# Optimization experiments

Hardware: AMD Instinct MI355X
Metric: run time of the kernel (lower is better)

Reference implementation:

```python
import jax, jax.numpy as jnp
import numpy as np

NUM_EXPERTS = 8
TOP_K = 2


def setup_inputs() -> dict:
    key = jax.random.key(0)
    k0, k1, k2, k3, k4 = jax.random.split(key, 5)
    sl, bs, hs, ffn = 2048, 2, 512, 2048
    T = sl * bs
    x = jax.random.normal(k0, (sl, bs, hs), jnp.float32)
    expert_weights = jax.random.uniform(k1, (T, TOP_K), jnp.float32)
    expert_indices = jax.random.randint(k2, (T, TOP_K), 0, NUM_EXPERTS)
    # per-expert MLP params (ParallelGroupedMLP, 'regular' mlp_type)
    w1 = jax.random.normal(k3, (NUM_EXPERTS, hs, ffn), jnp.float32) * (hs ** -0.5)
    w2 = jax.random.normal(k4, (NUM_EXPERTS, ffn, hs), jnp.float32) * (ffn ** -0.5)
    return dict(x=x, expert_weights=expert_weights, expert_indices=expert_indices, w1=w1, w2=w2)


def reference(x, expert_weights, expert_indices, w1, w2):
    """Dropless MoE: sort assignments by expert, gather tokens, grouped MLP,
    scatter-combine with top-k router weights (megablocks gather/scatter semantics)."""
    in_shape = x.shape
    hs = in_shape[-1]
    x_flat = x.reshape(-1, hs)                 # [T, hs]
    T = x_flat.shape[0]
    flat_ids = expert_indices.reshape(-1)      # [T*k] expert id per assignment
    order = jnp.argsort(flat_ids)              # indices: assignment order sorted by expert
    bin_ids = flat_ids[order]                  # expert id per sorted slot
    token_ids = order // TOP_K                 # source token per sorted slot
    xg = x_flat[token_ids]                     # gather: [T*k, hs]
    # grouped GEMM: fixed small loop over experts, mask-select per slot
    y = jnp.zeros_like(xg)
    for e in range(NUM_EXPERTS):
        h = jax.nn.gelu(xg @ w1[e], approximate=False)   # [T*k, ffn]
        y = jnp.where((bin_ids == e)[:, None], h @ w2[e], y)
    # scatter-combine: out[token] += weight[assignment] * y[slot]
    w = expert_weights.reshape(-1)[order][:, None]       # [T*k, 1]
    out = jnp.zeros((T, hs), x.dtype).at[token_ids].add(w * y)
    return out.reshape(in_shape)
```

## Files before the change

### kernel.cpp

```cpp
#include <hip/hip_runtime.h>
#include <stdint.h>

#define T_TOK 4096
#define KTOP  2
#define HS    512
#define FFN   2048
#define NE    8
#define NA    (T_TOK*KTOP)
#define MT    128
#define BK    64
#define MT_MAX 72
#define SLOT_CAP (MT_MAX*MT)
#define PSTR 68
#define NB_G1 576

#define MB_ (1024ull*1024ull)
#define WS_OFF   1024u
#define WS_MEXP  1088u
#define WS_SLOTS 2048u
#define WS_INV   40960u
#define WS_XB   (1*MB_)
#define WS_W1T  (5*MB_)
#define WS_W2T  (21*MB_)
#define WS_HB   (37*MB_)
#define WS_YPB0 (73*MB_)
#define WS_YPB1 (82*MB_)
#define WS_NEED (91*MB_)

typedef short bf16x8 __attribute__((ext_vector_type(8)));
typedef float f32x4  __attribute__((ext_vector_type(4)));

__device__ __forceinline__ unsigned short f2bf(float f) {
    unsigned u = __builtin_bit_cast(unsigned, f);
    u += 0x7fffu + ((u >> 16) & 1u);
    return (unsigned short)(u >> 16);
}
__device__ __forceinline__ float bf2f(unsigned short h) {
    return __builtin_bit_cast(float, (unsigned)h << 16);
}
__device__ __forceinline__ float gelu_fast(float x) {
    float x2 = x * x;
    float inner = fmaf(0.044715f * x2, x, x);
    float E = __expf(1.5957691216057308f * inner);
    return x - x / (1.0f + E);
}
__device__ __forceinline__ void gl_lds16(const void* g, void* l) {
    __builtin_amdgcn_global_load_lds(
        (const __attribute__((address_space(1))) unsigned int*)g,
        (__attribute__((address_space(3))) unsigned int*)l, 16, 0, 0);
}

__device__ __forceinline__ void transpose_cvt64(
    const float* __restrict__ src, unsigned short* __restrict__ dh,
    int R, int C, int e, int kb, int nb, int t, float (*tile)[65])
{
    const int k0 = kb * 64, n0 = nb * 64;
    #pragma unroll
    for (int q = 0; q < 4; ++q) {
        int f4 = t + q * 256;
        int kk = f4 >> 4, nn4 = f4 & 15;
        float4 v = *reinterpret_cast<const float4*>(
            &src[((size_t)e * R + k0 + kk) * C + n0 + nn4 * 4]);
        tile[kk][nn4 * 4 + 0] = v.x; tile[kk][nn4 * 4 + 1] = v.y;
        tile[kk][nn4 * 4 + 2] = v.z; tile[kk][nn4 * 4 + 3] = v.w;
    }
    __syncthreads();
    #pragma unroll
    for (int q = 0; q < 4; ++q) {
        int wid = t + q * 256;
        int nn = wid >> 4, kk4 = wid & 15;
        ushort4 o;
        o.x = f2bf(tile[kk4 * 4 + 0][nn]);
        o.y = f2bf(tile[kk4 * 4 + 1][nn]);
        o.z = f2bf(tile[kk4 * 4 + 2][nn]);
        o.w = f2bf(tile[kk4 * 4 + 3][nn]);
        *reinterpret_cast<ushort4*>(&dh[((size_t)e * C + n0 + nn) * R + k0 + kk4 * 4]) = o;
    }
}

__global__ void moe_prep1(const int* __restrict__ eidx,
                          int* slots, int* inv, int* offp, int* mexp,
                          const float* __restrict__ x, unsigned short* __restrict__ xb,
                          const float* __restrict__ w1, unsigned short* __restrict__ w1t)
{
    __shared__ float tile[64][65];
    const int bid = blockIdx.x, t = threadIdx.x;
    if (bid < 2048) {
        int i = bid * 256 + t;
        float4 v = reinterpret_cast<const float4*>(x)[i];
        uint2 p = { (unsigned)f2bf(v.x) | ((unsigned)f2bf(v.y) << 16),
                    (unsigned)f2bf(v.z) | ((unsigned)f2bf(v.w) << 16) };
        reinterpret_cast<uint2*>(xb)[i] = p;
    } else if (bid < 4096) {
        int lin = bid - 2048, e = lin >> 8, rem = lin & 255;
        transpose_cvt64(w1, w1t, HS, FFN, e, rem & 7, rem >> 3, t, tile);
    } else {
        __shared__ int hfull[NE], hpre[NE], elocal[256];
        __shared__ int off_l[NE + 1];
        const int f = bid - 4096;
        if (t < NE) { hfull[t] = 0; hpre[t] = 0; }
        __syncthreads();
        const int base = f * 256;
        for (int i = t; i < NA; i += 256) {
            int ee = eidx[i];
            atomicAdd(&hfull[ee], 1);
            if (i < base) atomicAdd(&hpre[ee], 1);
        }
        if (f < 32) elocal[t] = eidx[base + t];
        __syncthreads();
        if (t == 0) {
            int run = 0;
            for (int q = 0; q < NE; ++q) { off_l[q] = run; run += ((hfull[q] + MT - 1) / MT) * MT; }
            off_l[NE] = run;
        }
        __syncthreads();
        if (f < 32) {
            int a = base + t, e = elocal[t];
            int rank = 0;
            for (int j = 0; j < t; ++j) rank += (elocal[j] == e) ? 1 : 0;
            int s = off_l[e] + hpre[e] + rank;
            slots[s] = a;
            inv[a] = s;
        } else {
            for (int e = 0; e < NE; ++e)
                for (int s = off_l[e] + hfull[e] + t; s < off_l[e + 1]; s += 256)
                    slots[s] = -1;
            for (int s = off_l[NE] + t; s < SLOT_CAP; s += 256) slots[s] = -1;
            if (t <= NE) offp[t] = off_l[t];
            if (t < MT_MAX) {
                int m0 = t * MT, ee = 0;
                #pragma unroll
                for (int q = 0; q < NE; ++q)
                    if (m0 >= off_l[q] && m0 < off_l[q + 1]) ee = q;
                mexp[t] = ee;
            }
        }
    }
}

__global__ __launch_bounds__(256, 2) void moe_g1w2(
    const unsigned short* __restrict__ XB, const unsigned short* __restrict__ W1T,
    const int* __restrict__ offp, const int* __restrict__ mexp,
    const int* __restrict__ slots, unsigned short* __restrict__ HB,
    const float* __restrict__ w2, unsigned short* __restrict__ w2t)
{
    __shared__ __align__(16) char POOL[49152];
    __shared__ int srow[MT];
    const int t = threadIdx.x;

    if (blockIdx.x >= NB_G1) {
        int lin = blockIdx.x - NB_G1;
        int e = lin >> 8, rem = lin & 255;
        transpose_cvt64(w2, w2t, FFN, HS, e, rem & 31, rem >> 5, t,
                        reinterpret_cast<float(*)[65]>(POOL));
        return;
    }

    const int xcd = blockIdx.x & 7;
    const int part = blockIdx.x >> 3;
    const int mtg = part % 9;
    const int nt  = part / 9;
    const int mt  = xcd * 9 + mtg;
    if (mt * MT >= offp[NE]) return;
    const int e = mexp[mt];
    const int lane = t & 63, wv = t >> 6;

    short* As = (short*)POOL;
    short* Bs = (short*)(POOL + 16384);
    float* Pf = (float*)POOL;

    if (t < MT) { int s = slots[mt * MT + t]; srow[t] = (s < 0) ? 0 : (s >> 1); }
    __syncthreads();

    int baseA[4], baseB[8];
    #pragma unroll
    for (int q = 0; q < 4; ++q) {
        int i = wv * 4 + q;
        int row = i * 8 + (lane >> 3);
        int sg = (lane & 7) ^ (row & 7);
        baseA[q] = srow[row] * HS + sg * 8;
    }
    #pragma unroll
    for (int q = 0; q < 8; ++q) {
        int j = wv * 8 + q;
        int row = j * 8 + (lane >> 3);
        int sg = (lane & 7) ^ (row & 7);
        baseB[q] = (e * FFN + nt * 256 + row) * HS + sg * 8;
    }

    const int wm = wv >> 1, wn = wv & 1, q4 = lane >> 4, l15 = lane & 15;
    int offA[2][4], offB[2][8];
    #pragma unroll
    for (int m = 0; m < 4; ++m) {
        int r = wm * 64 + m * 16 + l15;
        #pragma unroll
        for (int ks = 0; ks < 2; ++ks)
            offA[ks][m] = r * 128 + ((((ks << 2) | q4) ^ (r & 7)) << 4);
    }
    #pragma unroll
    for (int n = 0; n < 8; ++n) {
        int rb = wn * 128 + n * 16 + l15;
        #pragma unroll
        for (int ks = 0; ks < 2; ++ks)
            offB[ks][n] = rb * 128 + ((((ks << 2) | q4) ^ (rb & 7)) << 4);
    }

    f32x4 acc[4][8];
    #pragma unroll
    for (int m = 0; m < 4; ++m)
        #pragma unroll
        for (int n = 0; n < 8; ++n) { f32x4 z = {0.f, 0.f, 0.f, 0.f}; acc[m][n] = z; }

    for (int kk = 0; kk < HS; kk += BK) {
        __syncthreads();
        #pragma unroll
        for (int q = 0; q < 4; ++q)
            gl_lds16(XB + baseA[q] + kk, (char*)As + (wv * 4 + q) * 1024);
        #pragma unroll
        for (int q = 0; q < 8; ++q)
            gl_lds16(W1T + baseB[q] + kk, (char*)Bs + (wv * 8 + q) * 1024);
        __syncthreads();
        #pragma unroll
        for (int ks = 0; ks < 2; ++ks) {
            bf16x8 a[4], b[8];
            #pragma unroll
            for (int m = 0; m < 4; ++m)
                a[m] = *(const bf16x8*)((const char*)As + offA[ks][m]);
            #pragma unroll
            for (int n = 0; n < 8; ++n)
                b[n] = *(const bf16x8*)((const char*)Bs + offB[ks][n]);
            #pragma unroll
            for (int m = 0; m < 4; ++m)
                #pragma unroll
                for (int n = 0; n < 8; ++n)
                    acc[m][n] = __builtin_amdgcn_mfma_f32_16x16x32_bf16(a[m], b[n], acc[m][n], 0, 0, 0);
        }
    }

    #pragma unroll
    for (int qq = 0; qq < 4; ++qq) {
        const int wn_q = qq >> 1, nq = (qq & 1) * 4;
        __syncthreads();
        if (wn == wn_q) {
            #pragma unroll
            for (int m = 0; m < 4; ++m)
                #pragma unroll
                for (int nn = 0; nn < 4; ++nn)
                    #pragma unroll
                    for (int j = 0; j < 4; ++j)
                        Pf[(wm * 64 + m * 16 + q4 * 4 + j) * PSTR + nn * 16 + l15] = acc[m][nq + nn][j];
        }
        __syncthreads();
        #pragma unroll
        for (int q = 0; q < 4; ++q) {
            int seg = q * 256 + t, row = seg >> 3, c8 = (seg & 7) << 3;
            const float* p = Pf + row * PSTR + c8;
            float4 a = *(const float4*)p, b = *(const float4*)(p + 4);
            float va[8] = {a.x, a.y, a.z, a.w, b.x, b.y, b.z, b.w};
            bf16x8 ph;
            #pragma unroll
            for (int i = 0; i < 8; ++i) ph[i] = (short)f2bf(gelu_fast(va[i]));
            *(bf16x8*)(HB + (size_t)(mt * MT + row) * FFN + nt * 256 + qq * 64 + c8) = ph;
        }
    }
}

__global__ __launch_bounds__(256, 4) void moe_gemm2(
    const unsigned short* __restrict__ HB, const unsigned short* __restrict__ W2T,
    const int* __restrict__ offp, const int* __restrict__ mexp,
    unsigned short* __restrict__ YPB0, unsigned short* __restrict__ YPB1)
{
    const int xcd = blockIdx.x & 7;
    const int part = blockIdx.x >> 3;
    const int sub = part % 8;
    const int mtg = part / 8;
    const int mt  = xcd * 9 + mtg;
    const int nt  = sub >> 1, kpart = sub & 1;
    if (mt * MT >= offp[NE]) return;
    const int e = mexp[mt];
    const int t = threadIdx.x, lane = t & 63, wv = t >> 6;

    __shared__ __align__(16) char POOL[MT * PSTR * 4];
    short* As = (short*)POOL;
    short* Bs = (short*)(POOL + 16384);
    float* Pf = (float*)POOL;

    int baseA[4], baseB[4];
    #pragma unroll
    for (int q = 0; q < 4; ++q) {
        int i = wv * 4 + q;
        int row = i * 8 + (lane >> 3);
        int sg = (lane & 7) ^ (row & 7);
        baseA[q] = (mt * MT + row) * FFN + sg * 8;
        baseB[q] = (e * HS + nt * MT + row) * FFN + sg * 8;
    }

    const int wm = wv >> 1, wn = wv & 1, q4 = lane >> 4, l15 = lane & 15;
    int offA[2][4], offB[2][4];
    #pragma unroll
    for (int m = 0; m < 4; ++m) {
        int r  = wm * 64 + m * 16 + l15;
        int rb = wn * 64 + m * 16 + l15;
        #pragma unroll
        for (int ks = 0; ks < 2; ++ks) {
            offA[ks][m] = r  * 128 + ((((ks << 2) | q4) ^ (r  & 7)) << 4);
            offB[ks][m] = rb * 128 + ((((ks << 2) | q4) ^ (rb & 7)) << 4);
        }
    }

    f32x4 acc[4][4];
    #pragma unroll
    for (int m = 0; m < 4; ++m)
        #pragma unroll
        for (int n = 0; n < 4; ++n) { f32x4 z = {0.f, 0.f, 0.f, 0.f}; acc[m][n] = z; }

    const int k0 = kpart * (FFN / 2), k1 = k0 + FFN / 2;
    for (int kk = k0; kk < k1; kk += BK) {
        __syncthreads();
        #pragma unroll
        for (int q = 0; q < 4; ++q) {
            int i = wv * 4 + q;
            gl_lds16(HB  + baseA[q] + kk, (char*)As + i * 1024);
            gl_lds16(W2T + baseB[q] + kk, (char*)Bs + i * 1024);
        }
        __syncthreads();
        #pragma unroll
        for (int ks = 0; ks < 2; ++ks) {
            bf16x8 a[4], b[4];
            #pragma unroll
            for (int m = 0; m < 4; ++m) {
                a[m] = *(const bf16x8*)((const char*)As + offA[ks][m]);
                b[m] = *(const bf16x8*)((const char*)Bs + offB[ks][m]);
            }
            #pragma unroll
            for (int m = 0; m < 4; ++m)
                #pragma unroll
                for (int n = 0; n < 4; ++n)
                    acc[m][n] = __builtin_amdgcn_mfma_f32_16x16x32_bf16(a[m], b[n], acc[m][n], 0, 0, 0);
        }
    }

    unsigned short* YP = kpart ? YPB1 : YPB0;
    #pragma unroll
    for (int half = 0; half < 2; ++half) {
        __syncthreads();
        if (wn == half) {
            #pragma unroll
            for (int m = 0; m < 4; ++m)
                #pragma unroll
                for (int n = 0; n < 4; ++n)
                    #pragma unroll
                    for (int j = 0; j < 4; ++j)
                        Pf[(wm * 64 + m * 16 + q4 * 4 + j) * PSTR + n * 16 + l15] = acc[m][n][j];
        }
        __syncthreads();
        #pragma unroll
        for (int q = 0; q < 4; ++q) {
            int seg = q * 256 + t, row = seg >> 3, c8 = (seg & 7) << 3;
            const float* p = Pf + row * PSTR + c8;
            float4 a = *(const float4*)p, b = *(const float4*)(p + 4);
            float va[8] = {a.x, a.y, a.z, a.w, b.x, b.y, b.z, b.w};
            bf16x8 ph;
            #pragma unroll
            for (int i = 0; i < 8; ++i) ph[i] = (short)f2bf(va[i]);
            *(bf16x8*)(YP + (size_t)(mt * MT + row) * HS + nt * MT + half * 64 + c8) = ph;
        }
    }
}

__global__ void moe_combine2(const unsigned short* __restrict__ YPB0,
                             const unsigned short* __restrict__ YPB1,
                             const int* __restrict__ inv, const float* __restrict__ ew,
                             float* __restrict__ out) {
    int i = blockIdx.x * 256 + threadIdx.x;
    if (i >= T_TOK * HS / 8) return;
    int tk = i >> 6, c8 = (i & 63) << 3;
    int s0 = inv[2 * tk], s1 = inv[2 * tk + 1];
    float w0 = ew[2 * tk], w1 = ew[2 * tk + 1];
    bf16x8 a0 = *(const bf16x8*)(YPB0 + (size_t)s0 * HS + c8);
    bf16x8 b0 = *(const bf16x8*)(YPB1 + (size_t)s0 * HS + c8);
    bf16x8 a1 = *(const bf16x8*)(YPB0 + (size_t)s1 * HS + c8);
    bf16x8 b1 = *(const bf16x8*)(YPB1 + (size_t)s1 * HS + c8);
    float o[8];
    #pragma unroll
    for (int j = 0; j < 8; ++j)
        o[j] = w0 * (bf2f((unsigned short)a0[j]) + bf2f((unsigned short)b0[j]))
             + w1 * (bf2f((unsigned short)a1[j]) + bf2f((unsigned short)b1[j]));
    float4* d = reinterpret_cast<float4*>(out + (size_t)i * 8);
    d[0] = make_float4(o[0], o[1], o[2], o[3]);
    d[1] = make_float4(o[4], o[5], o[6], o[7]);
}

#define FB_BM 32
#define FB_BJ 128
#define FB_CK 256
#define FB_XSTR (FB_CK+4)
#define FB_HSTR (FB_BJ+4)

__device__ __forceinline__ float fb_gelu(float v) {
    return 0.5f * v * (1.0f + erff(v * 0.70710678118654752f));
}

__global__ void fb_init(int* cnt) { int i = threadIdx.x; if (i < NE) cnt[i] = 0; }

__global__ void fb_scatter(const int* __restrict__ eidx, int* cnt, int* bucket) {
    int a = blockIdx.x * 256 + threadIdx.x;
    if (a < NA) { int e = eidx[a]; int p = atomicAdd(&cnt[e], 1); bucket[e * NA + p] = a; }
}

__global__ __launch_bounds__(256, 1) void fb_fused(
    const float* __restrict__ x, const float* __restrict__ w1, const float* __restrict__ w2,
    const int* __restrict__ cnt, const int* __restrict__ bucket, float* __restrict__ ybuf)
{
    const int bid = blockIdx.x;
    const int e = bid & (NE - 1), tr = bid >> 3;
    const int n_e = cnt[e], rbase = tr * FB_BM;
    if (rbase >= n_e) return;
    const int t = threadIdx.x;
    __shared__ __align__(16) float Xc[FB_BM][FB_XSTR];
    __shared__ __align__(16) float Hsh[FB_BM][FB_HSTR];
    __shared__ int rowa[FB_BM];
    if (t < FB_BM) { int r = rbase + t; rowa[t] = (r < n_e) ? bucket[e * NA + r] : -1; }
    __syncthreads();
    const int cg = t & 15, rg = t >> 4, r0 = rg * 2;
    float yac[2][32];
    #pragma unroll
    for (int u = 0; u < 2; ++u)
        #pragma unroll
        for (int v = 0; v < 32; ++v) yac[u][v] = 0.0f;
    const float* w1e = w1 + (size_t)e * HS * FFN;
    const float* w2e = w2 + (size_t)e * FFN * HS;
    for (int jp = 0; jp < FFN; jp += FB_BJ) {
        float hac[2][8];
        #pragma unroll
        for (int u = 0; u < 2; ++u)
            #pragma unroll
            for (int v = 0; v < 8; ++v) hac[u][v] = 0.0f;
        for (int ic = 0; ic < HS; ic += FB_CK) {
            __syncthreads();
            #pragma unroll
            for (int q = 0; q < (FB_BM * FB_CK / 4) / 256; ++q) {
                int id = t + 256 * q, rr = id >> 6, c4 = id & 63;
                int a = rowa[rr];
                float4 val = make_float4(0.f, 0.f, 0.f, 0.f);
                if (a >= 0) val = *reinterpret_cast<const float4*>(x + (size_t)(a >> 1) * HS + ic + c4 * 4);
                *reinterpret_cast<float4*>(&Xc[rr][c4 * 4]) = val;
            }
            __syncthreads();
            const float* w1p = w1e + (size_t)ic * FFN + jp + cg * 8;
            #pragma unroll 2
            for (int i4 = 0; i4 < FB_CK; i4 += 4) {
                float4 xa = *reinterpret_cast<const float4*>(&Xc[r0][i4]);
                float4 xb = *reinterpret_cast<const float4*>(&Xc[r0 + 1][i4]);
                const float* wr0 = w1p + (size_t)i4 * FFN;
                #pragma unroll
                for (int ii = 0; ii < 4; ++ii) {
                    float4 wa = *reinterpret_cast<const float4*>(wr0 + (size_t)ii * FFN);
                    float4 wb = *reinterpret_cast<const float4*>(wr0 + (size_t)ii * FFN + 4);
                    float x0 = (ii == 0) ? xa.x : (ii == 1) ? xa.y : (ii == 2) ? xa.z : xa.w;
                    float x1 = (ii == 0) ? xb.x : (ii == 1) ? xb.y : (ii == 2) ? xb.z : xb.w;
                    hac[0][0] = fmaf(x0, wa.x, hac[0][0]); hac[0][1] = fmaf(x0, wa.y, hac[0][1]);
                    hac[0][2] = fmaf(x0, wa.z, hac[0][2]); hac[0][3] = fmaf(x0, wa.w, hac[0][3]);
                    hac[0][4] = fmaf(x0, wb.x, hac[0][4]); hac[0][5] = fmaf(x0, wb.y, hac[0][5]);
                    hac[0][6] = fmaf(x0, wb.z, hac[0][6]); hac[0][7] = fmaf(x0, wb.w, hac[0][7]);
                    hac[1][0] = fmaf(x1, wa.x, hac[1][0]); hac[1][1] = fmaf(x1, wa.y, hac[1][1]);
                    hac[1][2] = fmaf(x1, wa.z, hac[1][2]); hac[1][3] = fmaf(x1, wa.w, hac[1][3]);
                    hac[1][4] = fmaf(x1, wb.x, hac[1][4]); hac[1][5] = fmaf(x1, wb.y, hac[1][5]);
                    hac[1][6] = fmaf(x1, wb.z, hac[1][6]); hac[1][7] = fmaf(x1, wb.w, hac[1][7]);
                }
            }
        }
        #pragma unroll
        for (int u = 0; u < 2; ++u)
            #pragma unroll
            for (int v = 0; v < 8; ++v) Hsh[r0 + u][cg * 8 + v] = fb_gelu(hac[u][v]);
        __syncthreads();
        const float* w2p = w2e + (size_t)jp * HS + cg * 32;
        #pragma unroll 2
        for (int j = 0; j < FB_BJ; ++j) {
            float h0 = Hsh[r0][j], h1 = Hsh[r0 + 1][j];
            const float* wr = w2p + (size_t)j * HS;
            #pragma unroll
            for (int q = 0; q < 8; ++q) {
                float4 w4 = *reinterpret_cast<const float4*>(wr + q * 4);
                yac[0][q * 4 + 0] = fmaf(h0, w4.x, yac[0][q * 4 + 0]);
                yac[0][q * 4 + 1] = fmaf(h0, w4.y, yac[0][q * 4 + 1]);
                yac[0][q * 4 + 2] = fmaf(h0, w4.z, yac[0][q * 4 + 2]);
                yac[0][q * 4 + 3] = fmaf(h0, w4.w, yac[0][q * 4 + 3]);
                yac[1][q * 4 + 0] = fmaf(h1, w4.x, yac[1][q * 4 + 0]);
                yac[1][q * 4 + 1] = fmaf(h1, w4.y, yac[1][q * 4 + 1]);
                yac[1][q * 4 + 2] = fmaf(h1, w4.z, yac[1][q * 4 + 2]);
                yac[1][q * 4 + 3] = fmaf(h1, w4.w, yac[1][q * 4 + 3]);
            }
        }
    }
    #pragma unroll
    for (int u = 0; u < 2; ++u) {
        int a = rowa[r0 + u];
        if (a >= 0) {
            float* yp = ybuf + (size_t)a * HS + cg * 32;
            #pragma unroll
            for (int q = 0; q < 8; ++q) {
                float4 o = make_float4(yac[u][q * 4 + 0], yac[u][q * 4 + 1],
                                       yac[u][q * 4 + 2], yac[u][q * 4 + 3]);
                *reinterpret_cast<float4*>(yp + q * 4) = o;
            }
        }
    }
}

__global__ void fb_combine(const float* __restrict__ ybuf, const float* __restrict__ ew,
                           float* __restrict__ out) {
    int i = blockIdx.x * 256 + threadIdx.x;
    if (i >= T_TOK * HS / 4) return;
    int tk = i >> 7, c4 = i & 127;
    float wA = ew[2 * tk], wB = ew[2 * tk + 1];
    const float4* y4 = reinterpret_cast<const float4*>(ybuf);
    float4 a = y4[(size_t)(2 * tk) * (HS / 4) + c4];
    float4 b = y4[(size_t)(2 * tk + 1) * (HS / 4) + c4];
    float4 o;
    o.x = wA * a.x + wB * b.x; o.y = wA * a.y + wB * b.y;
    o.z = wA * a.z + wB * b.z; o.w = wA * a.w + wB * b.w;
    reinterpret_cast<float4*>(out)[i] = o;
}

extern "C" void kernel_launch(void* const* d_in, const int* in_sizes, int n_in,
                              void* d_out, int out_size, void* d_ws, size_t ws_size,
                              hipStream_t stream) {
    const float* x  = (const float*)d_in[0];
    const float* ew = (const float*)d_in[1];
    const int*   ei = (const int*)d_in[2];
    const float* w1 = (const float*)d_in[3];
    const float* w2 = (const float*)d_in[4];
    float* out = (float*)d_out;
    char* W = (char*)d_ws;

    if (ws_size < WS_NEED) {
        int* cnt = (int*)d_ws;
        int* bucket = cnt + 64;
        float* ybuf = (float*)(W + (1 << 19));
        fb_init<<<1, 64, 0, stream>>>(cnt);
        fb_scatter<<<NA / 256, 256, 0, stream>>>(ei, cnt, bucket);
        fb_fused<<<NE * (NA / FB_BM), 256, 0, stream>>>(x, w1, w2, cnt, bucket, ybuf);
        fb_combine<<<(T_TOK * HS / 4 + 255) / 256, 256, 0, stream>>>(ybuf, ew, out);
        return;
    }

    int* offp  = (int*)(W + WS_OFF);
    int* mexp  = (int*)(W + WS_MEXP);
    int* slots = (int*)(W + WS_SLOTS);
    int* inv   = (int*)(W + WS_INV);
    unsigned short* XB   = (unsigned short*)(W + WS_XB);
    unsigned short* W1T  = (unsigned short*)(W + WS_W1T);
    unsigned short* W2T  = (unsigned short*)(W + WS_W2T);
    unsigned short* HB   = (unsigned short*)(W + WS_HB);
    unsigned short* YPB0 = (unsigned short*)(W + WS_YPB0);
    unsigned short* YPB1 = (unsigned short*)(W + WS_YPB1);

    moe_prep1<<<4129, 256, 0, stream>>>(ei, slots, inv, offp, mexp, x, XB, w1, W1T);
    moe_g1w2<<<NB_G1 + 2048, 256, 0, stream>>>(XB, W1T, offp, mexp, slots, HB, w2, W2T);
    moe_gemm2<<<8 * 9 * 8, 256, 0, stream>>>(HB, W2T, offp, mexp, YPB0, YPB1);
    moe_combine2<<<(T_TOK * HS / 8) / 256, 256, 0, stream>>>(YPB0, YPB1, inv, ew, out);
}
```

Before: 101.8 us.

## Retile grouped GEMMs: smaller GEMM1 N-tile, drop GEMM2 split-K

GEMM1 tiles shrink from 128x256 to 128x128, which doubles its block count and lets it run at higher occupancy with a smaller LDS pool. GEMM2 no longer splits K into two partial-output buffers. Each block now computes a 128x64 tile over the full FFN reduction and writes one bf16 result, so the combine kernel reads half as many buffers and skips the partial-sum add. The aim is better load balance and occupancy and less partial-output traffic. In exchange, each GEMM2 block runs a longer serial K loop and GEMM1 reuses operands less per tile.

```diff
diff --git a/kernel.cpp b/kernel.cpp
--- a/kernel.cpp
+++ b/kernel.cpp
@@ -12,7 +12,7 @@
 #define MT_MAX 72
 #define SLOT_CAP (MT_MAX*MT)
 #define PSTR 68
-#define NB_G1 576
+#define NB_G1 1152
 
 #define MB_ (1024ull*1024ull)
 #define WS_OFF   1024u
@@ -23,9 +23,8 @@
 #define WS_W1T  (5*MB_)
 #define WS_W2T  (21*MB_)
 #define WS_HB   (37*MB_)
-#define WS_YPB0 (73*MB_)
-#define WS_YPB1 (82*MB_)
-#define WS_NEED (91*MB_)
+#define WS_YB   (73*MB_)
+#define WS_NEED (82*MB_)
 
 typedef short bf16x8 __attribute__((ext_vector_type(8)));
 typedef float f32x4  __attribute__((ext_vector_type(4)));
@@ -138,13 +137,13 @@
     }
 }
 
-__global__ __launch_bounds__(256, 2) void moe_g1w2(
+__global__ __launch_bounds__(256, 4) void moe_g1w2(
     const unsigned short* __restrict__ XB, const unsigned short* __restrict__ W1T,
     const int* __restrict__ offp, const int* __restrict__ mexp,
     const int* __restrict__ slots, unsigned short* __restrict__ HB,
     const float* __restrict__ w2, unsigned short* __restrict__ w2t)
 {
-    __shared__ __align__(16) char POOL[49152];
+    __shared__ __align__(16) char POOL[MT * PSTR * 4];
     __shared__ int srow[MT];
     const int t = threadIdx.x;
 
@@ -172,83 +171,71 @@
     if (t < MT) { int s = slots[mt * MT + t]; srow[t] = (s < 0) ? 0 : (s >> 1); }
     __syncthreads();
 
-    int baseA[4], baseB[8];
+    int baseA[4], baseB[4];
     #pragma unroll
     for (int q = 0; q < 4; ++q) {
         int i = wv * 4 + q;
         int row = i * 8 + (lane >> 3);
         int sg = (lane & 7) ^ (row & 7);
         baseA[q] = srow[row] * HS + sg * 8;
-    }
-    #pragma unroll
-    for (int q = 0; q < 8; ++q) {
-        int j = wv * 8 + q;
-        int row = j * 8 + (lane >> 3);
-        int sg = (lane & 7) ^ (row & 7);
-        baseB[q] = (e * FFN + nt * 256 + row) * HS + sg * 8;
+        baseB[q] = (e * FFN + nt * MT + row) * HS + sg * 8;
     }
 
     const int wm = wv >> 1, wn = wv & 1, q4 = lane >> 4, l15 = lane & 15;
-    int offA[2][4], offB[2][8];
+    int offA[2][4], offB[2][4];
     #pragma unroll
     for (int m = 0; m < 4; ++m) {
-        int r = wm * 64 + m * 16 + l15;
-        #pragma unroll
-        for (int ks = 0; ks < 2; ++ks)
-            offA[ks][m] = r * 128 + ((((ks << 2) | q4) ^ (r & 7)) << 4);
-    }
-    #pragma unroll
-    for (int n = 0; n < 8; ++n) {
-        int rb = wn * 128 + n * 16 + l15;
-        #pragma unroll
-        for (int ks = 0; ks < 2; ++ks)
-            offB[ks][n] = rb * 128 + ((((ks << 2) | q4) ^ (rb & 7)) << 4);
-    }
-
-    f32x4 acc[4][8];
+        int r  = wm * 64 + m * 16 + l15;
+        int rb = wn * 64 + m * 16 + l15;
+        #pragma unroll
+        for (int ks = 0; ks < 2; ++ks) {
+            offA[ks][m] = r  * 128 + ((((ks << 2) | q4) ^ (r  & 7)) << 4);
+            offB[ks][m] = rb * 128 + ((((ks << 2) | q4) ^ (rb & 7)) << 4);
+        }
+    }
+
+    f32x4 acc[4][4];
     #pragma unroll
     for (int m = 0; m < 4; ++m)
         #pragma unroll
-        for (int n = 0; n < 8; ++n) { f32x4 z = {0.f, 0.f, 0.f, 0.f}; acc[m][n] = z; }
+        for (int n = 0; n < 4; ++n) { f32x4 z = {0.f, 0.f, 0.f, 0.f}; acc[m][n] = z; }
 
     for (int kk = 0; kk < HS; kk += BK) {
         __syncthreads();
         #pragma unroll
-        for (int q = 0; q < 4; ++q)
-            gl_lds16(XB + baseA[q] + kk, (char*)As + (wv * 4 + q) * 1024);
-        #pragma unroll
-        for (int q = 0; q < 8; ++q)
-            gl_lds16(W1T + baseB[q] + kk, (char*)Bs + (wv * 8 + q) * 1024);
+        for (int q = 0; q < 4; ++q) {
+            int i = wv * 4 + q;
+            gl_lds16(XB  + baseA[q] + kk, (char*)As + i * 1024);
+            gl_lds16(W1T + baseB[q] + kk, (char*)Bs + i * 1024);
+        }
         __syncthreads();
         #pragma unroll
         for (int ks = 0; ks < 2; ++ks) {
-            bf16x8 a[4], b[8];
-            #pragma unroll
-            for (int m = 0; m < 4; ++m)
+            bf16x8 a[4], b[4];
+            #pragma unroll
+            for (int m = 0; m < 4; ++m) {
                 a[m] = *(const bf16x8*)((const char*)As + offA[ks][m]);
-            #pragma unroll
-            for (int n = 0; n < 8; ++n)
-                b[n] = *(const bf16x8*)((const char*)Bs + offB[ks][n]);
+                b[m] = *(const bf16x8*)((const char*)Bs + offB[ks][m]);
+            }
             #pragma unroll
             for (int m = 0; m < 4; ++m)
                 #pragma unroll
-                for (int n = 0; n < 8; ++n)
+                for (int n = 0; n < 4; ++n)
                     acc[m][n] = __builtin_amdgcn_mfma_f32_16x16x32_bf16(a[m], b[n], acc[m][n], 0, 0, 0);
         }
     }
 
     #pragma unroll
-    for (int qq = 0; qq < 4; ++qq) {
-        const int wn_q = qq >> 1, nq = (qq & 1) * 4;
-        __syncthreads();
-        if (wn == wn_q) {
+    for (int half = 0; half < 2; ++half) {
+        __syncthreads();
+        if (wn == half) {
             #pragma unroll
             for (int m = 0; m < 4; ++m)
                 #pragma unroll
-                for (int nn = 0; nn < 4; ++nn)
+                for (int n = 0; n < 4; ++n)
                     #pragma unroll
                     for (int j = 0; j < 4; ++j)
-                        Pf[(wm * 64 + m * 16 + q4 * 4 + j) * PSTR + nn * 16 + l15] = acc[m][nq + nn][j];
+                        Pf[(wm * 64 + m * 16 + q4 * 4 + j) * PSTR + n * 16 + l15] = acc[m][n][j];
         }
         __syncthreads();
         #pragma unroll
@@ -260,116 +247,126 @@
             bf16x8 ph;
             #pragma unroll
             for (int i = 0; i < 8; ++i) ph[i] = (short)f2bf(gelu_fast(va[i]));
-            *(bf16x8*)(HB + (size_t)(mt * MT + row) * FFN + nt * 256 + qq * 64 + c8) = ph;
-        }
-    }
-}
-
-__global__ __launch_bounds__(256, 4) void moe_gemm2(
+            *(bf16x8*)(HB + (size_t)(mt * MT + row) * FFN + nt * MT + half * 64 + c8) = ph;
+        }
+    }
+}
+
+__global__ __launch_bounds__(256, 6) void moe_gemm2(
     const unsigned short* __restrict__ HB, const unsigned short* __restrict__ W2T,
     const int* __restrict__ offp, const int* __restrict__ mexp,
-    unsigned short* __restrict__ YPB0, unsigned short* __restrict__ YPB1)
+    unsigned short* __restrict__ YB)
 {
     const int xcd = blockIdx.x & 7;
     const int part = blockIdx.x >> 3;
     const int sub = part % 8;
     const int mtg = part / 8;
     const int mt  = xcd * 9 + mtg;
-    const int nt  = sub >> 1, kpart = sub & 1;
     if (mt * MT >= offp[NE]) return;
     const int e = mexp[mt];
     const int t = threadIdx.x, lane = t & 63, wv = t >> 6;
 
-    __shared__ __align__(16) char POOL[MT * PSTR * 4];
+    __shared__ __align__(16) char POOL[24576];
     short* As = (short*)POOL;
     short* Bs = (short*)(POOL + 16384);
     float* Pf = (float*)POOL;
 
-    int baseA[4], baseB[4];
+    int baseA[4], baseB[2];
     #pragma unroll
     for (int q = 0; q < 4; ++q) {
         int i = wv * 4 + q;
         int row = i * 8 + (lane >> 3);
         int sg = (lane & 7) ^ (row & 7);
         baseA[q] = (mt * MT + row) * FFN + sg * 8;
-        baseB[q] = (e * HS + nt * MT + row) * FFN + sg * 8;
+    }
+    #pragma unroll
+    for (int q = 0; q < 2; ++q) {
+        int i = wv * 2 + q;
+        int row = i * 8 + (lane >> 3);
+        int sg = (lane & 7) ^ (row & 7);
+        baseB[q] = (e * HS + sub * 64 + row) * FFN + sg * 8;
     }
 
     const int wm = wv >> 1, wn = wv & 1, q4 = lane >> 4, l15 = lane & 15;
-    int offA[2][4], offB[2][4];
+    int offA[2][4], offB[2][2];
     #pragma unroll
     for (int m = 0; m < 4; ++m) {
-        int r  = wm * 64 + m * 16 + l15;
-        int rb = wn * 64 + m * 16 + l15;
+        int r = wm * 64 + m * 16 + l15;
+        #pragma unroll
+        for (int ks = 0; ks < 2; ++ks)
+            offA[ks][m] = r * 128 + ((((ks << 2) | q4) ^ (r & 7)) << 4);
+    }
+    #pragma unroll
+    for (int n = 0; n < 2; ++n) {
+        int rb = wn * 32 + n * 16 + l15;
+        #pragma unroll
+        for (int ks = 0; ks < 2; ++ks)
+            offB[ks][n] = rb * 128 + ((((ks << 2) | q4) ^ (rb & 7)) << 4);
+    }
+
+    f32x4 acc[4][2];
+    #pragma unroll
+    for (int m = 0; m < 4; ++m)
+        #pragma unroll
+        for (int n = 0; n < 2; ++n) { f32x4 z = {0.f, 0.f, 0.f, 0.f}; acc[m][n] = z; }
+
+    for (int kk = 0; kk < FFN; kk += BK) {
+        __syncthreads();
+        #pragma unroll
+        for (int q = 0; q < 4; ++q)
+            gl_lds16(HB + baseA[q] + kk, (char*)As + (wv * 4 + q) * 1024);
+        #pragma unroll
+        for (int q = 0; q < 2; ++q)
+            gl_lds16(W2T + baseB[q] + kk, (char*)Bs + (wv * 2 + q) * 1024);
+        __syncthreads();
         #pragma unroll
         for (int ks = 0; ks < 2; ++ks) {
-            offA[ks][m] = r  * 128 + ((((ks << 2) | q4) ^ (r  & 7)) << 4);
-            offB[ks][m] = rb * 128 + ((((ks << 2) | q4) ^ (rb & 7)) << 4);
-        }
-    }
-
-    f32x4 acc[4][4];
-    #pragma unroll
-    for (int m = 0; m < 4; ++m)
-        #pragma unroll
-        for (int n = 0; n < 4; ++n) { f32x4 z = {0.f, 0.f, 0.f, 0.f}; acc[m][n] = z; }
-
-    const int k0 = kpart * (FFN / 2), k1 = k0 + FFN / 2;
-    for (int kk = k0; kk < k1; kk += BK) {
-        __syncthreads();
-        #pragma unroll
-        for (int q = 0; q < 4; ++q) {
-            int i = wv * 4 + q;
-            gl_lds16(HB  + baseA[q] + kk, (char*)As + i * 1024);
-            gl_lds16(W2T + baseB[q] + kk, (char*)Bs + i * 1024);
-        }
-        __syncthreads();
-        #pragma unroll
-        for (int ks = 0; ks < 2; ++ks) {
-            bf16x8 a[4], b[4];
-            #pragma unroll
-            for (int m = 0; m < 4; ++m) {
+            bf16x8 a[4], b[2];
+            #pragma unroll
+            for (int m = 0; m < 4; ++m)
                 a[m] = *(const bf16x8*)((const char*)As + offA[ks][m]);
-                b[m] = *(const bf16x8*)((const char*)Bs + offB[ks][m]);
-            }
+            #pragma unroll
+            for (int n = 0; n < 2; ++n)
+                b[n] = *(const bf16x8*)((const char*)Bs + offB[ks][n]);
             #pragma unroll
             for (int m = 0; m < 4; ++m)
                 #pragma unroll
-                for (int n = 0; n < 4; ++n)
+                for (int n = 0; n < 2; ++n)
                     acc[m][n] = __builtin_amdgcn_mfma_f32_16x16x32_bf16(a[m], b[n], acc[m][n], 0, 0, 0);
         }
     }
 
-    unsigned short* YP = kpart ? YPB1 : YPB0;
-    #pragma unroll
-    for (int half = 0; half < 2; ++half) {
-        __syncthreads();
-        if (wn == half) {
+    #pragma unroll
+    for (int rh = 0; rh < 2; ++rh) {
+        __syncthreads();
+        if (wm == rh) {
             #pragma unroll
             for (int m = 0; m < 4; ++m)
                 #pragma unroll
-                for (int n = 0; n < 4; ++n)
+                for (int n = 0; n < 2; ++n)
                     #pragma unroll
                     for (int j = 0; j < 4; ++j)
-                        Pf[(wm * 64 + m * 16 + q4 * 4 + j) * PSTR + n * 16 + l15] = acc[m][n][j];
-        }
-        __syncthreads();
-        #pragma unroll
-        for (int q = 0; q < 4; ++q) {
-            int seg = q * 256 + t, row = seg >> 3, c8 = (seg & 7) << 3;
-            const float* p = Pf + row * PSTR + c8;
-            float4 a = *(const float4*)p, b = *(const float4*)(p + 4);
-            float va[8] = {a.x, a.y, a.z, a.w, b.x, b.y, b.z, b.w};
-            bf16x8 ph;
-            #pragma unroll
-            for (int i = 0; i < 8; ++i) ph[i] = (short)f2bf(va[i]);
-            *(bf16x8*)(YP + (size_t)(mt * MT + row) * HS + nt * MT + half * 64 + c8) = ph;
-        }
-    }
-}
-
-__global__ void moe_combine2(const unsigned short* __restrict__ YPB0,
-                             const unsigned short* __restrict__ YPB1,
+                        Pf[(m * 16 + q4 * 4 + j) * PSTR + wn * 32 + n * 16 + l15] = acc[m][n][j];
+        }
+        __syncthreads();
+        {
+            int row = t >> 2, c16 = (t & 3) * 16;
+            const float* p = Pf + row * PSTR + c16;
+            float4 a = *(const float4*)p,      b = *(const float4*)(p + 4);
+            float4 c = *(const float4*)(p + 8), d = *(const float4*)(p + 12);
+            float va[16] = {a.x, a.y, a.z, a.w, b.x, b.y, b.z, b.w,
+                            c.x, c.y, c.z, c.w, d.x, d.y, d.z, d.w};
+            bf16x8 p0, p1;
+            #pragma unroll
+            for (int i = 0; i < 8; ++i) { p0[i] = (short)f2bf(va[i]); p1[i] = (short)f2bf(va[8 + i]); }
+            unsigned short* dst = YB + (size_t)(mt * MT + rh * 64 + row) * HS + sub * 64 + c16;
+            *(bf16x8*)dst = p0;
+            *(bf16x8*)(dst + 8) = p1;
+        }
+    }
+}
+
+__global__ void moe_combine2(const unsigned short* __restrict__ YB,
                              const int* __restrict__ inv, const float* __restrict__ ew,
                              float* __restrict__ out) {
     int i = blockIdx.x * 256 + threadIdx.x;
@@ -377,15 +374,12 @@
     int tk = i >> 6, c8 = (i & 63) << 3;
     int s0 = inv[2 * tk], s1 = inv[2 * tk + 1];
     float w0 = ew[2 * tk], w1 = ew[2 * tk + 1];
-    bf16x8 a0 = *(const bf16x8*)(YPB0 + (size_t)s0 * HS + c8);
-    bf16x8 b0 = *(const bf16x8*)(YPB1 + (size_t)s0 * HS + c8);
-    bf16x8 a1 = *(const bf16x8*)(YPB0 + (size_t)s1 * HS + c8);
-    bf16x8 b1 = *(const bf16x8*)(YPB1 + (size_t)s1 * HS + c8);
+    bf16x8 a0 = *(const bf16x8*)(YB + (size_t)s0 * HS + c8);
+    bf16x8 a1 = *(const bf16x8*)(YB + (size_t)s1 * HS + c8);
     float o[8];
     #pragma unroll
     for (int j = 0; j < 8; ++j)
-        o[j] = w0 * (bf2f((unsigned short)a0[j]) + bf2f((unsigned short)b0[j]))
-             + w1 * (bf2f((unsigned short)a1[j]) + bf2f((unsigned short)b1[j]));
+        o[j] = w0 * bf2f((unsigned short)a0[j]) + w1 * bf2f((unsigned short)a1[j]);
     float4* d = reinterpret_cast<float4*>(out + (size_t)i * 8);
     d[0] = make_float4(o[0], o[1], o[2], o[3]);
     d[1] = make_float4(o[4], o[5], o[6], o[7]);
@@ -554,11 +548,10 @@
     unsigned short* W1T  = (unsigned short*)(W + WS_W1T);
     unsigned short* W2T  = (unsigned short*)(W + WS_W2T);
     unsigned short* HB   = (unsigned short*)(W + WS_HB);
-    unsigned short* YPB0 = (unsigned short*)(W + WS_YPB0);
-    unsigned short* YPB1 = (unsigned short*)(W + WS_YPB1);
+    unsigned short* YB   = (unsigned short*)(W + WS_YB);
 
     moe_prep1<<<4129, 256, 0, stream>>>(ei, slots, inv, offp, mexp, x, XB, w1, W1T);
     moe_g1w2<<<NB_G1 + 2048, 256, 0, stream>>>(XB, W1T, offp, mexp, slots, HB, w2, W2T);
-    moe_gemm2<<<8 * 9 * 8, 256, 0, stream>>>(HB, W2T, offp, mexp, YPB0, YPB1);
-    moe_combine2<<<(T_TOK * HS / 8) / 256, 256, 0, stream>>>(YPB0, YPB1, inv, ew, out);
-}
+    moe_gemm2<<<8 * 9 * 8, 256, 0, stream>>>(HB, W2T, offp, mexp, YB);
+    moe_combine2<<<(T_TOK * HS / 8) / 256, 256, 0, stream>>>(YB, inv, ew, out);
+}
```

After: 98.15 us. 3.6% less time.
